# Optimization experiments

Measured on AMD Instinct MI355X. Metric: run time of the kernel, lower is better.

The kernel has to match this reference:

```python
import jax, jax.numpy as jnp
import numpy as np

ALPHA = 0.2          # LeakyReLU negative slope
NEG_FILL = -9e15     # mask value used by the original module


def setup_inputs() -> dict:
    key = jax.random.key(0)
    k1, k2, k3, k4 = jax.random.split(key, 4)
    N, D, H, F = 4096, 512, 8, 64  # nhid*nheads == embedding_dim
    h = jax.random.normal(k1, (N, D), dtype=jnp.float32)
    adj = jax.random.randint(k2, (N, N), 0, 2, dtype=jnp.int32)
    # per-head linear projection weights (no bias) and attention vectors
    W = jax.random.normal(k3, (H, D, F), dtype=jnp.float32) * (1.0 / np.sqrt(D))
    a = jax.random.normal(k4, (H, 2 * F), dtype=jnp.float32) * 0.1
    return {"h": h, "adj": adj, "W": W, "a": a}


def reference(h, adj, W, a):
    H, D, F = W.shape
    N = h.shape[0]
    # per-head projection: [H, N, F]
    hp = jnp.einsum('nd,hdf->hnf', h, W)
    # score(i,j) = leakyrelu(a[:F].h_i + a[F:].h_j)  (decomposed broadcast-add,
    # same math as the original N*N concat construction)
    a_src, a_dst = a[:, :F], a[:, F:]
    f_src = jnp.einsum('hnf,hf->hn', hp, a_src)  # [H, N]
    f_dst = jnp.einsum('hnf,hf->hn', hp, a_dst)  # [H, N]
    e = jax.nn.leaky_relu(f_src[:, :, None] + f_dst[:, None, :], ALPHA)  # [H,N,N]
    e = jnp.where(adj[None] > 0, e, NEG_FILL)
    att = jax.nn.softmax(e, axis=-1)  # softmax over neighbors j (dim=1 in torch)
    out = jnp.einsum('hij,hjf->hif', att, hp)  # [H, N, F]
    # concat heads -> [N, H*F], then ELU
    out = jnp.transpose(out, (1, 0, 2)).reshape(N, H * F)
    return jax.nn.elu(out)
```

## Files before the change

### kernel.cpp

```cpp
#include <hip/hip_runtime.h>

#define NN 4096
#define DD 512
#define HH 8
#define FF 64
#define LRELU_ALPHA 0.2f
#define SP 72
#define JSPLIT 2
#define JCHUNK (NN / JSPLIT)

typedef __attribute__((ext_vector_type(8))) short bf16x8;
typedef __attribute__((ext_vector_type(4))) float f32x4;

__device__ __forceinline__ float f4c(const float4& v, int k) {
    return k == 0 ? v.x : (k == 1 ? v.y : (k == 2 ? v.z : v.w));
}
__device__ __forceinline__ void f4s(float4& v, int k, float x) {
    if (k == 0) v.x = x; else if (k == 1) v.y = x; else if (k == 2) v.z = x; else v.w = x;
}
__device__ __forceinline__ unsigned short f2bf(float x) {
    unsigned u = __float_as_uint(x);
    return (unsigned short)((u + 0x7fffu + ((u >> 16) & 1u)) >> 16);
}
__device__ __forceinline__ float bf2f(unsigned short h) {
    return __uint_as_float(((unsigned)h) << 16);
}
__device__ __forceinline__ unsigned fkey(float x) {
    unsigned u = __float_as_uint(x);
    return (u & 0x80000000u) ? ~u : (u | 0x80000000u);
}
__device__ __forceinline__ float funkey(unsigned k) {
    unsigned u = (k & 0x80000000u) ? (k ^ 0x80000000u) : ~k;
    return __uint_as_float(u);
}

__global__ __launch_bounds__(256) void k_prep(const int* __restrict__ adj,
                                              const float* __restrict__ W,
                                              const float* __restrict__ hmat,
                                              unsigned long long* __restrict__ adjm,
                                              unsigned short* __restrict__ wt_hi,
                                              unsigned short* __restrict__ wt_lo,
                                              unsigned short* __restrict__ h_hi,
                                              unsigned short* __restrict__ h_lo,
                                              unsigned* __restrict__ mxkey,
                                              float* __restrict__ hpsum) {
    __shared__ unsigned long long shbuf[2080];
    int b = blockIdx.x, t = threadIdx.x;
    if (b < 2048) {
        int g = b >> 3, cs = b & 7;
        int r0 = g * 16;
        int lane = t & 63, wv = t >> 6;
        unsigned long long (*w64)[9] = (unsigned long long(*)[9])shbuf;
        for (int r = 0; r < 16; r++) {
            #pragma unroll
            for (int q = 0; q < 2; q++) {
                int col = cs * 512 + q * 256 + t;
                unsigned long long m = __ballot(adj[(size_t)(r0 + r) * NN + col] > 0);
                if (lane == 0) w64[r][q * 4 + wv] = m;
            }
        }
        __syncthreads();
        for (int tl = wv; tl < 8; tl += 4) {
            unsigned long long wbits = w64[lane & 15][tl];
            unsigned long long my = 0;
            #pragma unroll
            for (int k = 0; k < 16; k++) {
                int shv = 32 * (k >> 3) + 8 * (lane >> 4) + (k & 7);
                unsigned long long bal = __ballot((unsigned)((wbits >> shv) & 1ULL));
                if (lane == k) my = bal;
            }
            if (lane < 16)
                adjm[((size_t)g * 64 + cs * 8 + tl) * 16 + lane] = my;
        }
    } else if (b < 2112) {
        float (*tile)[65] = (float(*)[65])shbuf;
        int idx = b - 2048;
        int h = idx >> 3;
        int d0 = (idx & 7) * 64;
        #pragma unroll
        for (int kidx = 0; kidx < 4; kidx++) {
            int id = t + 256 * kidx;
            int dd = id >> 4, f4i = (id & 15) * 4;
            float4 v = *(const float4*)(W + ((size_t)(h * DD + d0 + dd)) * FF + f4i);
            tile[dd][f4i] = v.x; tile[dd][f4i + 1] = v.y;
            tile[dd][f4i + 2] = v.z; tile[dd][f4i + 3] = v.w;
        }
        __syncthreads();
        int f = t >> 2, c = (t & 3) * 16;
        union { unsigned short s[16]; uint4 v[2]; } hb, lb;
        #pragma unroll
        for (int q = 0; q < 16; q++) {
            float v = tile[c + q][f];
            unsigned short hi = f2bf(v);
            hb.s[q] = hi;
            lb.s[q] = f2bf(v - bf2f(hi));
        }
        uint4* dh = (uint4*)(wt_hi + ((size_t)h * FF + f) * DD + d0 + c);
        uint4* dl = (uint4*)(wt_lo + ((size_t)h * FF + f) * DD + d0 + c);
        dh[0] = hb.v[0]; dh[1] = hb.v[1];
        dl[0] = lb.v[0]; dl[1] = lb.v[1];
    } else if (b < 2368) {
        int idx = b - 2112;
        int row = idx * 16 + (t >> 4);
        int c0 = (t & 15) * 32;
        const float* src = hmat + (size_t)row * DD + c0;
        #pragma unroll
        for (int half = 0; half < 2; half++) {
            float4 p0 = *(const float4*)(src + half * 16);
            float4 p1 = *(const float4*)(src + half * 16 + 4);
            float4 p2 = *(const float4*)(src + half * 16 + 8);
            float4 p3 = *(const float4*)(src + half * 16 + 12);
            union { unsigned short s[16]; uint4 v[2]; } hb, lb;
            #pragma unroll
            for (int q = 0; q < 16; q++) {
                float v = q < 4 ? f4c(p0, q) : q < 8 ? f4c(p1, q - 4)
                          : q < 12 ? f4c(p2, q - 8) : f4c(p3, q - 12);
                unsigned short hi = f2bf(v);
                hb.s[q] = hi;
                lb.s[q] = f2bf(v - bf2f(hi));
            }
            uint4* dh = (uint4*)(h_hi + (size_t)row * DD + c0 + half * 16);
            uint4* dl = (uint4*)(h_lo + (size_t)row * DD + c0 + half * 16);
            dh[0] = hb.v[0]; dh[1] = hb.v[1];
            dl[0] = lb.v[0]; dl[1] = lb.v[1];
        }
    } else {
        if (t < 16) mxkey[t] = 0u;
        hpsum[t] = 0.f;
        hpsum[t + 256] = 0.f;
    }
}

__global__ __launch_bounds__(256) void k_hp_mfma(const unsigned short* __restrict__ hhi,
                                                 const unsigned short* __restrict__ hlo,
                                                 const unsigned short* __restrict__ whi,
                                                 const unsigned short* __restrict__ wlo,
                                                 const float* __restrict__ a,
                                                 unsigned short* __restrict__ hpT_hi,
                                                 float* __restrict__ fs,
                                                 float* __restrict__ fd,
                                                 float* __restrict__ hpsum,
                                                 unsigned* __restrict__ mxkey) {
    __shared__ char smem[4 * 64 * SP * 2];
    unsigned short* ah = (unsigned short*)smem;
    unsigned short* al = ah + 64 * SP;
    unsigned short* bh = al + 64 * SP;
    unsigned short* bl = bh + 64 * SP;

    int t = threadIdx.x;
    int h = blockIdx.y;
    int n0 = blockIdx.x * 64;
    int lane = t & 63;
    int w = t >> 6;
    int R0 = (w >> 1) * 32, F0 = (w & 1) * 32;
    int am = lane & 15, aq = lane >> 4;
    int sr = t >> 2, sc = (t & 3) * 16;

    const unsigned short* ghh = hhi + (size_t)(n0 + sr) * DD;
    const unsigned short* ghl = hlo + (size_t)(n0 + sr) * DD;
    const unsigned short* gbh = whi + ((size_t)h * FF + sr) * DD;
    const unsigned short* gbl = wlo + ((size_t)h * FF + sr) * DD;

    f32x4 acc[2][2] = {};
    for (int kk = 0; kk < DD; kk += 64) {
        {
            const uint4* s0 = (const uint4*)(ghh + kk + sc);
            const uint4* s1 = (const uint4*)(ghl + kk + sc);
            uint4 h0 = s0[0], h1 = s0[1], l0 = s1[0], l1 = s1[1];
            *(uint4*)(ah + sr * SP + sc) = h0; *(uint4*)(ah + sr * SP + sc + 8) = h1;
            *(uint4*)(al + sr * SP + sc) = l0; *(uint4*)(al + sr * SP + sc + 8) = l1;
        }
        {
            const uint4* s2 = (const uint4*)(gbh + kk + sc);
            const uint4* s3 = (const uint4*)(gbl + kk + sc);
            uint4 w0 = s2[0], w1 = s2[1], x0 = s3[0], x1 = s3[1];
            *(uint4*)(bh + sr * SP + sc) = w0; *(uint4*)(bh + sr * SP + sc + 8) = w1;
            *(uint4*)(bl + sr * SP + sc) = x0; *(uint4*)(bl + sr * SP + sc + 8) = x1;
        }
        __syncthreads();
        #pragma unroll
        for (int k2 = 0; k2 < 2; k2++) {
            int ko = k2 * 32 + aq * 8;
            bf16x8 a0h = *(const bf16x8*)(ah + (R0 + am) * SP + ko);
            bf16x8 a1h = *(const bf16x8*)(ah + (R0 + 16 + am) * SP + ko);
            bf16x8 a0l = *(const bf16x8*)(al + (R0 + am) * SP + ko);
            bf16x8 a1l = *(const bf16x8*)(al + (R0 + 16 + am) * SP + ko);
            bf16x8 b0h = *(const bf16x8*)(bh + (F0 + am) * SP + ko);
            bf16x8 b1h = *(const bf16x8*)(bh + (F0 + 16 + am) * SP + ko);
            bf16x8 b0l = *(const bf16x8*)(bl + (F0 + am) * SP + ko);
            bf16x8 b1l = *(const bf16x8*)(bl + (F0 + 16 + am) * SP + ko);
            acc[0][0] = __builtin_amdgcn_mfma_f32_16x16x32_bf16(a0h, b0h, acc[0][0], 0, 0, 0);
            acc[0][1] = __builtin_amdgcn_mfma_f32_16x16x32_bf16(a0h, b1h, acc[0][1], 0, 0, 0);
            acc[1][0] = __builtin_amdgcn_mfma_f32_16x16x32_bf16(a1h, b0h, acc[1][0], 0, 0, 0);
            acc[1][1] = __builtin_amdgcn_mfma_f32_16x16x32_bf16(a1h, b1h, acc[1][1], 0, 0, 0);
            acc[0][0] = __builtin_amdgcn_mfma_f32_16x16x32_bf16(a0h, b0l, acc[0][0], 0, 0, 0);
            acc[0][1] = __builtin_amdgcn_mfma_f32_16x16x32_bf16(a0h, b1l, acc[0][1], 0, 0, 0);
            acc[1][0] = __builtin_amdgcn_mfma_f32_16x16x32_bf16(a1h, b0l, acc[1][0], 0, 0, 0);
            acc[1][1] = __builtin_amdgcn_mfma_f32_16x16x32_bf16(a1h, b1l, acc[1][1], 0, 0, 0);
            acc[0][0] = __builtin_amdgcn_mfma_f32_16x16x32_bf16(a0l, b0h, acc[0][0], 0, 0, 0);
            acc[0][1] = __builtin_amdgcn_mfma_f32_16x16x32_bf16(a0l, b1h, acc[0][1], 0, 0, 0);
            acc[1][0] = __builtin_amdgcn_mfma_f32_16x16x32_bf16(a1l, b0h, acc[1][0], 0, 0, 0);
            acc[1][1] = __builtin_amdgcn_mfma_f32_16x16x32_bf16(a1l, b1h, acc[1][1], 0, 0, 0);
        }
        __syncthreads();
    }

    unsigned* tt = (unsigned*)smem;
    float* rs = (float*)(smem + 17408);
    float* rd = rs + 256;
    float* ash = rd + 256;
    if (t < 128) ash[t] = a[h * 2 * FF + t];
    int col = lane & 15, rbase = (lane >> 4) * 4;
    #pragma unroll
    for (int m16 = 0; m16 < 2; m16++) {
        #pragma unroll
        for (int n16 = 0; n16 < 2; n16++) {
            #pragma unroll
            for (int r = 0; r < 4; r++) {
                int nl = R0 + m16 * 16 + rbase + r;
                int f = F0 + n16 * 16 + col;
                float v = acc[m16][n16][r];
                unsigned short hi = f2bf(v);
                unsigned short lo = f2bf(v - bf2f(hi));
                tt[f * 68 + nl] = (unsigned)hi | ((unsigned)lo << 16);
            }
        }
    }
    __syncthreads();
    {
        int f = t >> 2, c = (t & 3) * 16;
        union { unsigned short s[16]; uint4 v[2]; } hb;
        float csum = 0.f;
        #pragma unroll
        for (int q = 0; q < 16; q++) {
            unsigned u = tt[f * 68 + c + q];
            hb.s[q] = (unsigned short)(u & 0xffffu);
            csum += bf2f((unsigned short)(u & 0xffffu)) + bf2f((unsigned short)(u >> 16));
        }
        uint4* dh = (uint4*)(hpT_hi + ((size_t)h * FF + f) * NN + n0 + c);
        dh[0] = hb.v[0]; dh[1] = hb.v[1];
        csum += __shfl_xor(csum, 1);
        csum += __shfl_xor(csum, 2);
        if ((t & 3) == 0) unsafeAtomicAdd(hpsum + h * FF + f, csum);
    }
    {
        int n = t & 63, g = t >> 6;
        float fsp = 0.f, fdp = 0.f;
        #pragma unroll
        for (int q = 0; q < 16; q++) {
            int f = g * 16 + q;
            unsigned u = tt[f * 68 + n];
            float v = bf2f((unsigned short)(u & 0xffffu)) + bf2f((unsigned short)(u >> 16));
            fsp += v * ash[f];
            fdp += v * ash[64 + f];
        }
        rs[g * 64 + n] = fsp;
        rd[g * 64 + n] = fdp;
    }
    __syncthreads();
    if (t < 64) {
        const float LOG2E = 1.44269504f;
        float fdv = (rd[t] + rd[64 + t] + rd[128 + t] + rd[192 + t]) * LOG2E;
        fs[(size_t)h * NN + n0 + t] = (rs[t] + rs[64 + t] + rs[128 + t] + rs[192 + t]) * LOG2E;
        fd[(size_t)h * NN + n0 + t] = fdv;
        unsigned key = fkey(fdv);
        #pragma unroll
        for (int off = 32; off; off >>= 1) key = max(key, (unsigned)__shfl_xor((int)key, off));
        if (t == 0) atomicMax(mxkey + h, key);
    }
}

__global__ __launch_bounds__(512) void k_attn(const float* __restrict__ fs,
                                              const float* __restrict__ fd,
                                              const unsigned* __restrict__ mxkey,
                                              const unsigned long long* __restrict__ adjm,
                                              const unsigned short* __restrict__ hpT_hi,
                                              const float* __restrict__ hpsum,
                                              float* __restrict__ outp) {
    __shared__ unsigned short hbh[2][2][64 * SP];

    int t = threadIdx.x;
    int h = blockIdx.y;
    int i0 = blockIdx.x * 64;
    int lane = t & 63;
    int w = t >> 6;
    int h2 = w >> 2;
    int rg = w & 3;
    int am = lane & 15, aq = lane >> 4;
    int th = t >> 8;
    int ts = t & 255;
    int sr = ts >> 2, sc = (ts & 3) * 16;

    float mfdL = funkey(mxkey[h]);
    float fsv = fs[(size_t)h * NN + i0 + rg * 16 + am];
    float sL = fsv + mfdL;
    float mrL = fmaxf(sL, LRELU_ALPHA * sL);
    float Ai = fsv - mrL;
    float Ci = -0.8f * mrL;

    int rgu = __builtin_amdgcn_readfirstlane(rg);
    int h2u = __builtin_amdgcn_readfirstlane(h2);
    const unsigned long long* mbase = adjm + ((size_t)(blockIdx.x * 4 + rgu) * 64) * 16;
    const unsigned short* gH = hpT_hi + (size_t)h * FF * NN;
    const float* fdh = fd + (size_t)h * NN + (size_t)h2u * JCHUNK;

    f32x4 acc[4] = {};
    f32x4 accl = {};
    bf16x8 ones;
    #pragma unroll
    for (int i = 0; i < 8; i++) ones[i] = (short)0x3f80;

    auto stage_load = [&](int j0, uint4& v0, uint4& v1) {
        const uint4* s = (const uint4*)(gH + (size_t)sr * NN + th * JCHUNK + j0 + sc);
        v0 = s[0]; v1 = s[1];
    };
    auto stage_write = [&](int buf, uint4 v0, uint4 v1) {
        *(uint4*)(&hbh[buf][th][sr * SP + sc]) = v0;
        *(uint4*)(&hbh[buf][th][sr * SP + sc + 8]) = v1;
    };
    auto fd_load = [&](int j0, float4* p) {
        p[0] = *(const float4*)(fdh + j0 + aq * 8);
        p[1] = *(const float4*)(fdh + j0 + aq * 8 + 4);
        p[2] = *(const float4*)(fdh + j0 + 32 + aq * 8);
        p[3] = *(const float4*)(fdh + j0 + 32 + aq * 8 + 4);
    };
    auto mkfrag = [&](float4 p0, float4 p1, const unsigned long long* mk, int off) -> bf16x8 {
        unsigned eu[8];
        #pragma unroll
        for (int q = 0; q < 2; q++) {
            float4 pv = q ? p1 : p0;
            #pragma unroll
            for (int bq = 0; bq < 4; bq++) {
                float tv = Ai + f4c(pv, bq);
                float uv = __builtin_fmaf(LRELU_ALPHA, tv, Ci);
                float ev = __builtin_amdgcn_exp2f(fmaxf(tv, uv));
                unsigned r;
                asm("v_cndmask_b32 %0, 0, %1, %2"
                    : "=v"(r) : "v"(ev), "s"(mk[off + q * 4 + bq]));
                eu[q * 4 + bq] = r;
            }
        }
        union { unsigned u[4]; bf16x8 v; } pk;
        pk.u[0] = __builtin_amdgcn_perm(eu[1], eu[0], 0x07060302);
        pk.u[1] = __builtin_amdgcn_perm(eu[3], eu[2], 0x07060302);
        pk.u[2] = __builtin_amdgcn_perm(eu[5], eu[4], 0x07060302);
        pk.u[3] = __builtin_amdgcn_perm(eu[7], eu[6], 0x07060302);
        return pk.v;
    };

    bf16x8 Pc0, Pc1;
    {
        uint4 v0, v1; float4 pf[4];
        stage_load(0, v0, v1);
        fd_load(0, pf);
        unsigned long long mk[16];
        #pragma unroll
        for (int k = 0; k < 16; k++) mk[k] = mbase[(size_t)(h2u * 32) * 16 + k];
        Pc0 = mkfrag(pf[0], pf[1], mk, 0);
        Pc1 = mkfrag(pf[2], pf[3], mk, 8);
        stage_write(0, v0, v1);
        __syncthreads();
    }

    for (int j0 = 0; j0 < JCHUNK; j0 += 64) {
        int cur = (j0 >> 6) & 1;
        int jn = (j0 + 64) & (JCHUNK - 1);
        uint4 v0, v1; float4 pf[4];
        stage_load(jn, v0, v1);
        fd_load(jn, pf);
        unsigned long long mk[16];
        #pragma unroll
        for (int k = 0; k < 16; k++) mk[k] = mbase[(size_t)(h2u * 32 + (jn >> 6)) * 16 + k];

        #pragma unroll
        for (int k2 = 0; k2 < 2; k2++) {
            int ko = k2 * 32 + aq * 8;
            bf16x8 x0 = *(const bf16x8*)(&hbh[cur][h2][(am)      * SP + ko]);
            bf16x8 x1 = *(const bf16x8*)(&hbh[cur][h2][(am + 16) * SP + ko]);
            bf16x8 x2 = *(const bf16x8*)(&hbh[cur][h2][(am + 32) * SP + ko]);
            bf16x8 x3 = *(const bf16x8*)(&hbh[cur][h2][(am + 48) * SP + ko]);
            bf16x8 P = k2 ? Pc1 : Pc0;
            acc[0] = __builtin_amdgcn_mfma_f32_16x16x32_bf16(x0, P, acc[0], 0, 0, 0);
            acc[1] = __builtin_amdgcn_mfma_f32_16x16x32_bf16(x1, P, acc[1], 0, 0, 0);
            acc[2] = __builtin_amdgcn_mfma_f32_16x16x32_bf16(x2, P, acc[2], 0, 0, 0);
            acc[3] = __builtin_amdgcn_mfma_f32_16x16x32_bf16(x3, P, acc[3], 0, 0, 0);
            accl   = __builtin_amdgcn_mfma_f32_16x16x32_bf16(ones, P, accl, 0, 0, 0);
        }

        stage_write(cur ^ 1, v0, v1);
        Pc0 = mkfrag(pf[0], pf[1], mk, 0);
        Pc1 = mkfrag(pf[2], pf[3], mk, 8);
        __syncthreads();
    }

    float* cb = (float*)hbh;
    if (h2 == 1) {
        #pragma unroll
        for (int mf = 0; mf < 4; mf++)
            *(f32x4*)&cb[((rg * 4 + mf) * 64 + lane) * 4] = acc[mf];
        cb[4096 + rg * 64 + lane] = accl[0];
    }
    __syncthreads();
    if (h2 == 0) {
        #pragma unroll
        for (int mf = 0; mf < 4; mf++) {
            f32x4 o = *(const f32x4*)&cb[((rg * 4 + mf) * 64 + lane) * 4];
            acc[mf] += o;
        }
        float li = accl[0] + cb[4096 + rg * 64 + lane];
        const float invN = 1.0f / NN;
        float rl = 1.f / li;
        int row = i0 + rg * 16 + am;
        float* orow = outp + (size_t)row * (HH * FF) + h * FF;
        #pragma unroll
        for (int mf = 0; mf < 4; mf++) {
            float4 ov;
            #pragma unroll
            for (int r = 0; r < 4; r++) {
                int f = mf * 16 + aq * 4 + r;
                float v;
                if (li > 0.f) v = acc[mf][r] * rl;
                else          v = hpsum[h * FF + f] * invN;
                v = v > 0.f ? v : __expf(v) - 1.f;
                f4s(ov, r, v);
            }
            *(float4*)(orow + mf * 16 + aq * 4) = ov;
        }
    }
}

extern "C" void kernel_launch(void* const* d_in, const int* in_sizes, int n_in,
                              void* d_out, int out_size, void* d_ws, size_t ws_size,
                              hipStream_t stream) {
    const float* hmat = (const float*)d_in[0];
    const int*   adj  = (const int*)d_in[1];
    const float* W    = (const float*)d_in[2];
    const float* a    = (const float*)d_in[3];
    float* out = (float*)d_out;

    char* ws = (char*)d_ws;
    unsigned short* hpT_hi = (unsigned short*)(ws);
    unsigned long long* adjm = (unsigned long long*)(ws + (4u << 20));
    unsigned short* wt_hi  = (unsigned short*)(ws + (6u << 20));
    unsigned short* wt_lo  = (unsigned short*)(ws + (6u << 20) + (512u << 10));
    float* fs    = (float*)(ws + (7u << 20));
    float* fd    = (float*)(ws + (7u << 20) + (128u << 10));
    unsigned* mxkey = (unsigned*)(ws + (7u << 20) + (256u << 10));
    float* hpsum = (float*)(mxkey + 16);
    unsigned short* h_hi = (unsigned short*)(ws + (8u << 20));
    unsigned short* h_lo = (unsigned short*)(ws + (12u << 20));

    k_prep   <<<dim3(2369),          256, 0, stream>>>(adj, W, hmat, adjm, wt_hi, wt_lo,
                                                       h_hi, h_lo, mxkey, hpsum);
    k_hp_mfma<<<dim3(64, 8),         256, 0, stream>>>(h_hi, h_lo, wt_hi, wt_lo, a,
                                                       hpT_hi, fs, fd, hpsum, mxkey);
    k_attn   <<<dim3(NN / 64, HH),   512, 0, stream>>>(fs, fd, mxkey, adjm,
                                                       hpT_hi, hpsum, out);
}
```

Measured before the change: 175.2 us.

## Split attention over j across two grid slices and combine partials in a new kernel

```diff
diff --git a/kernel.cpp b/kernel.cpp
--- a/kernel.cpp
+++ b/kernel.cpp
@@ -6,8 +6,7 @@
 #define FF 64
 #define LRELU_ALPHA 0.2f
 #define SP 72
-#define JSPLIT 2
-#define JCHUNK (NN / JSPLIT)
+#define JH 1024
 
 typedef __attribute__((ext_vector_type(8))) short bf16x8;
 typedef __attribute__((ext_vector_type(4))) float f32x4;
@@ -275,13 +274,15 @@
                                               const unsigned* __restrict__ mxkey,
                                               const unsigned long long* __restrict__ adjm,
                                               const unsigned short* __restrict__ hpT_hi,
-                                              const float* __restrict__ hpsum,
-                                              float* __restrict__ outp) {
+                                              float* __restrict__ outp,
+                                              float* __restrict__ poacc,
+                                              float* __restrict__ pli) {
     __shared__ unsigned short hbh[2][2][64 * SP];
 
     int t = threadIdx.x;
     int h = blockIdx.y;
     int i0 = blockIdx.x * 64;
+    int z = blockIdx.z;
     int lane = t & 63;
     int w = t >> 6;
     int h2 = w >> 2;
@@ -302,7 +303,7 @@
     int h2u = __builtin_amdgcn_readfirstlane(h2);
     const unsigned long long* mbase = adjm + ((size_t)(blockIdx.x * 4 + rgu) * 64) * 16;
     const unsigned short* gH = hpT_hi + (size_t)h * FF * NN;
-    const float* fdh = fd + (size_t)h * NN + (size_t)h2u * JCHUNK;
+    const float* fdh = fd + (size_t)h * NN + (size_t)z * 2048 + (size_t)h2u * JH;
 
     f32x4 acc[4] = {};
     f32x4 accl = {};
@@ -311,7 +312,7 @@
     for (int i = 0; i < 8; i++) ones[i] = (short)0x3f80;
 
     auto stage_load = [&](int j0, uint4& v0, uint4& v1) {
-        const uint4* s = (const uint4*)(gH + (size_t)sr * NN + th * JCHUNK + j0 + sc);
+        const uint4* s = (const uint4*)(gH + (size_t)sr * NN + z * 2048 + th * JH + j0 + sc);
         v0 = s[0]; v1 = s[1];
     };
     auto stage_write = [&](int buf, uint4 v0, uint4 v1) {
@@ -354,23 +355,25 @@
         stage_load(0, v0, v1);
         fd_load(0, pf);
         unsigned long long mk[16];
-        #pragma unroll
-        for (int k = 0; k < 16; k++) mk[k] = mbase[(size_t)(h2u * 32) * 16 + k];
+        size_t jt = (size_t)(z * 32 + h2u * 16) * 16;
+        #pragma unroll
+        for (int k = 0; k < 16; k++) mk[k] = mbase[jt + k];
         Pc0 = mkfrag(pf[0], pf[1], mk, 0);
         Pc1 = mkfrag(pf[2], pf[3], mk, 8);
         stage_write(0, v0, v1);
         __syncthreads();
     }
 
-    for (int j0 = 0; j0 < JCHUNK; j0 += 64) {
+    for (int j0 = 0; j0 < JH; j0 += 64) {
         int cur = (j0 >> 6) & 1;
-        int jn = (j0 + 64) & (JCHUNK - 1);
+        int jn = (j0 + 64) & (JH - 1);
         uint4 v0, v1; float4 pf[4];
         stage_load(jn, v0, v1);
         fd_load(jn, pf);
         unsigned long long mk[16];
-        #pragma unroll
-        for (int k = 0; k < 16; k++) mk[k] = mbase[(size_t)(h2u * 32 + (jn >> 6)) * 16 + k];
+        size_t jt = (size_t)(z * 32 + h2u * 16 + (jn >> 6)) * 16;
+        #pragma unroll
+        for (int k = 0; k < 16; k++) mk[k] = mbase[jt + k];
 
         #pragma unroll
         for (int k2 = 0; k2 < 2; k2++) {
@@ -408,25 +411,42 @@
             acc[mf] += o;
         }
         float li = accl[0] + cb[4096 + rg * 64 + lane];
-        const float invN = 1.0f / NN;
+        int row = i0 + rg * 16 + am;
+        float* dst = (z == 0) ? outp : poacc;
+        float* drow = dst + (size_t)row * (HH * FF) + h * FF;
+        #pragma unroll
+        for (int mf = 0; mf < 4; mf++)
+            *(f32x4*)(drow + mf * 16 + aq * 4) = acc[mf];
+        if (aq == 0) pli[(size_t)z * NN * HH + (size_t)row * HH + h] = li;
+    }
+}
+
+__global__ __launch_bounds__(256) void k_comb(float* __restrict__ outp,
+                                              const float* __restrict__ poacc,
+                                              const float* __restrict__ pli,
+                                              const float* __restrict__ hpsum) {
+    int gid = blockIdx.x * 256 + threadIdx.x;
+    const float invN = 1.0f / NN;
+    float4 v0 = ((const float4*)outp)[gid];
+    float4 v1 = ((const float4*)poacc)[gid];
+    int rh = gid >> 4;
+    int h = rh & (HH - 1);
+    int f0 = (gid & 15) * 4;
+    float li = pli[rh] + pli[NN * HH + rh];
+    float4 o;
+    if (li > 0.f) {
         float rl = 1.f / li;
-        int row = i0 + rg * 16 + am;
-        float* orow = outp + (size_t)row * (HH * FF) + h * FF;
-        #pragma unroll
-        for (int mf = 0; mf < 4; mf++) {
-            float4 ov;
-            #pragma unroll
-            for (int r = 0; r < 4; r++) {
-                int f = mf * 16 + aq * 4 + r;
-                float v;
-                if (li > 0.f) v = acc[mf][r] * rl;
-                else          v = hpsum[h * FF + f] * invN;
-                v = v > 0.f ? v : __expf(v) - 1.f;
-                f4s(ov, r, v);
-            }
-            *(float4*)(orow + mf * 16 + aq * 4) = ov;
-        }
-    }
+        o.x = (v0.x + v1.x) * rl; o.y = (v0.y + v1.y) * rl;
+        o.z = (v0.z + v1.z) * rl; o.w = (v0.w + v1.w) * rl;
+    } else {
+        o.x = hpsum[h * FF + f0]     * invN; o.y = hpsum[h * FF + f0 + 1] * invN;
+        o.z = hpsum[h * FF + f0 + 2] * invN; o.w = hpsum[h * FF + f0 + 3] * invN;
+    }
+    o.x = o.x > 0.f ? o.x : __expf(o.x) - 1.f;
+    o.y = o.y > 0.f ? o.y : __expf(o.y) - 1.f;
+    o.z = o.z > 0.f ? o.z : __expf(o.z) - 1.f;
+    o.w = o.w > 0.f ? o.w : __expf(o.w) - 1.f;
+    ((float4*)outp)[gid] = o;
 }
 
 extern "C" void kernel_launch(void* const* d_in, const int* in_sizes, int n_in,
@@ -447,13 +467,16 @@
     float* fd    = (float*)(ws + (7u << 20) + (128u << 10));
     unsigned* mxkey = (unsigned*)(ws + (7u << 20) + (256u << 10));
     float* hpsum = (float*)(mxkey + 16);
+    float* pli   = (float*)(ws + (7u << 20) + (384u << 10));
     unsigned short* h_hi = (unsigned short*)(ws + (8u << 20));
     unsigned short* h_lo = (unsigned short*)(ws + (12u << 20));
-
-    k_prep   <<<dim3(2369),          256, 0, stream>>>(adj, W, hmat, adjm, wt_hi, wt_lo,
-                                                       h_hi, h_lo, mxkey, hpsum);
-    k_hp_mfma<<<dim3(64, 8),         256, 0, stream>>>(h_hi, h_lo, wt_hi, wt_lo, a,
-                                                       hpT_hi, fs, fd, hpsum, mxkey);
-    k_attn   <<<dim3(NN / 64, HH),   512, 0, stream>>>(fs, fd, mxkey, adjm,
-                                                       hpT_hi, hpsum, out);
-}
+    float* poacc = (float*)(ws + (8u << 20));
+
+    k_prep   <<<dim3(2369),            256, 0, stream>>>(adj, W, hmat, adjm, wt_hi, wt_lo,
+                                                         h_hi, h_lo, mxkey, hpsum);
+    k_hp_mfma<<<dim3(64, 8),           256, 0, stream>>>(h_hi, h_lo, wt_hi, wt_lo, a,
+                                                         hpT_hi, fs, fd, hpsum, mxkey);
+    k_attn   <<<dim3(NN / 64, HH, 2),  512, 0, stream>>>(fs, fd, mxkey, adjm,
+                                                         hpT_hi, out, poacc, pli);
+    k_comb   <<<dim3(NN * HH * FF / 1024), 256, 0, stream>>>(out, poacc, pli, hpsum);
+}
```

Result: slower. 192.5 us (+9.9%).

## Factor softmax exponentials into per-node terms and deepen attention prefetch pipeline

Applied to the files above, without the earlier changes.

```diff
diff --git a/kernel.cpp b/kernel.cpp
--- a/kernel.cpp
+++ b/kernel.cpp
@@ -6,8 +6,7 @@
 #define FF 64
 #define LRELU_ALPHA 0.2f
 #define SP 72
-#define JSPLIT 2
-#define JCHUNK (NN / JSPLIT)
+#define JCHUNK 2048
 
 typedef __attribute__((ext_vector_type(8))) short bf16x8;
 typedef __attribute__((ext_vector_type(4))) float f32x4;
@@ -138,7 +137,8 @@
                                                  const float* __restrict__ a,
                                                  unsigned short* __restrict__ hpT_hi,
                                                  float* __restrict__ fs,
-                                                 float* __restrict__ fd,
+                                                 float* __restrict__ ejs,
+                                                 float* __restrict__ fjs,
                                                  float* __restrict__ hpsum,
                                                  unsigned* __restrict__ mxkey) {
     __shared__ char smem[4 * 64 * SP * 2];
@@ -262,7 +262,8 @@
         const float LOG2E = 1.44269504f;
         float fdv = (rd[t] + rd[64 + t] + rd[128 + t] + rd[192 + t]) * LOG2E;
         fs[(size_t)h * NN + n0 + t] = (rs[t] + rs[64 + t] + rs[128 + t] + rs[192 + t]) * LOG2E;
-        fd[(size_t)h * NN + n0 + t] = fdv;
+        ejs[(size_t)h * NN + n0 + t] = __builtin_amdgcn_exp2f(fdv);
+        fjs[(size_t)h * NN + n0 + t] = __builtin_amdgcn_exp2f(LRELU_ALPHA * fdv);
         unsigned key = fkey(fdv);
         #pragma unroll
         for (int off = 32; off; off >>= 1) key = max(key, (unsigned)__shfl_xor((int)key, off));
@@ -271,7 +272,8 @@
 }
 
 __global__ __launch_bounds__(512) void k_attn(const float* __restrict__ fs,
-                                              const float* __restrict__ fd,
+                                              const float* __restrict__ ejs,
+                                              const float* __restrict__ fjs,
                                               const unsigned* __restrict__ mxkey,
                                               const unsigned long long* __restrict__ adjm,
                                               const unsigned short* __restrict__ hpT_hi,
@@ -295,14 +297,15 @@
     float fsv = fs[(size_t)h * NN + i0 + rg * 16 + am];
     float sL = fsv + mfdL;
     float mrL = fmaxf(sL, LRELU_ALPHA * sL);
-    float Ai = fsv - mrL;
-    float Ci = -0.8f * mrL;
+    float EA = __builtin_amdgcn_exp2f(fsv - mrL);
+    float EC = __builtin_amdgcn_exp2f(LRELU_ALPHA * fsv - mrL);
 
     int rgu = __builtin_amdgcn_readfirstlane(rg);
     int h2u = __builtin_amdgcn_readfirstlane(h2);
     const unsigned long long* mbase = adjm + ((size_t)(blockIdx.x * 4 + rgu) * 64) * 16;
     const unsigned short* gH = hpT_hi + (size_t)h * FF * NN;
-    const float* fdh = fd + (size_t)h * NN + (size_t)h2u * JCHUNK;
+    const float* ejh = ejs + (size_t)h * NN + (size_t)h2u * JCHUNK;
+    const float* fjh = fjs + (size_t)h * NN + (size_t)h2u * JCHUNK;
 
     f32x4 acc[4] = {};
     f32x4 accl = {};
@@ -318,25 +321,28 @@
         *(uint4*)(&hbh[buf][th][sr * SP + sc]) = v0;
         *(uint4*)(&hbh[buf][th][sr * SP + sc + 8]) = v1;
     };
-    auto fd_load = [&](int j0, float4* p) {
-        p[0] = *(const float4*)(fdh + j0 + aq * 8);
-        p[1] = *(const float4*)(fdh + j0 + aq * 8 + 4);
-        p[2] = *(const float4*)(fdh + j0 + 32 + aq * 8);
-        p[3] = *(const float4*)(fdh + j0 + 32 + aq * 8 + 4);
+    auto ejf_load = [&](int j0, float4* pe, float4* pf) {
+        pe[0] = *(const float4*)(ejh + j0 + aq * 8);
+        pe[1] = *(const float4*)(ejh + j0 + aq * 8 + 4);
+        pe[2] = *(const float4*)(ejh + j0 + 32 + aq * 8);
+        pe[3] = *(const float4*)(ejh + j0 + 32 + aq * 8 + 4);
+        pf[0] = *(const float4*)(fjh + j0 + aq * 8);
+        pf[1] = *(const float4*)(fjh + j0 + aq * 8 + 4);
+        pf[2] = *(const float4*)(fjh + j0 + 32 + aq * 8);
+        pf[3] = *(const float4*)(fjh + j0 + 32 + aq * 8 + 4);
     };
-    auto mkfrag = [&](float4 p0, float4 p1, const unsigned long long* mk, int off) -> bf16x8 {
+    auto mkfrag = [&](const float4* pe, const float4* pf,
+                      const unsigned long long* mk, int off) -> bf16x8 {
         unsigned eu[8];
         #pragma unroll
         for (int q = 0; q < 2; q++) {
-            float4 pv = q ? p1 : p0;
+            float4 ev4 = pe[q], fv4 = pf[q];
             #pragma unroll
             for (int bq = 0; bq < 4; bq++) {
-                float tv = Ai + f4c(pv, bq);
-                float uv = __builtin_fmaf(LRELU_ALPHA, tv, Ci);
-                float ev = __builtin_amdgcn_exp2f(fmaxf(tv, uv));
+                float e = fmaxf(EA * f4c(ev4, bq), EC * f4c(fv4, bq));
                 unsigned r;
                 asm("v_cndmask_b32 %0, 0, %1, %2"
-                    : "=v"(r) : "v"(ev), "s"(mk[off + q * 4 + bq]));
+                    : "=v"(r) : "v"(e), "s"(mk[off + q * 4 + bq]));
                 eu[q * 4 + bq] = r;
             }
         }
@@ -347,31 +353,7 @@
         pk.u[3] = __builtin_amdgcn_perm(eu[7], eu[6], 0x07060302);
         return pk.v;
     };
-
-    bf16x8 Pc0, Pc1;
-    {
-        uint4 v0, v1; float4 pf[4];
-        stage_load(0, v0, v1);
-        fd_load(0, pf);
-        unsigned long long mk[16];
-        #pragma unroll
-        for (int k = 0; k < 16; k++) mk[k] = mbase[(size_t)(h2u * 32) * 16 + k];
-        Pc0 = mkfrag(pf[0], pf[1], mk, 0);
-        Pc1 = mkfrag(pf[2], pf[3], mk, 8);
-        stage_write(0, v0, v1);
-        __syncthreads();
-    }
-
-    for (int j0 = 0; j0 < JCHUNK; j0 += 64) {
-        int cur = (j0 >> 6) & 1;
-        int jn = (j0 + 64) & (JCHUNK - 1);
-        uint4 v0, v1; float4 pf[4];
-        stage_load(jn, v0, v1);
-        fd_load(jn, pf);
-        unsigned long long mk[16];
-        #pragma unroll
-        for (int k = 0; k < 16; k++) mk[k] = mbase[(size_t)(h2u * 32 + (jn >> 6)) * 16 + k];
-
+    auto consume = [&](int cur, bf16x8 P0, bf16x8 P1) {
         #pragma unroll
         for (int k2 = 0; k2 < 2; k2++) {
             int ko = k2 * 32 + aq * 8;
@@ -379,18 +361,64 @@
             bf16x8 x1 = *(const bf16x8*)(&hbh[cur][h2][(am + 16) * SP + ko]);
             bf16x8 x2 = *(const bf16x8*)(&hbh[cur][h2][(am + 32) * SP + ko]);
             bf16x8 x3 = *(const bf16x8*)(&hbh[cur][h2][(am + 48) * SP + ko]);
-            bf16x8 P = k2 ? Pc1 : Pc0;
+            bf16x8 P = k2 ? P1 : P0;
             acc[0] = __builtin_amdgcn_mfma_f32_16x16x32_bf16(x0, P, acc[0], 0, 0, 0);
             acc[1] = __builtin_amdgcn_mfma_f32_16x16x32_bf16(x1, P, acc[1], 0, 0, 0);
             acc[2] = __builtin_amdgcn_mfma_f32_16x16x32_bf16(x2, P, acc[2], 0, 0, 0);
             acc[3] = __builtin_amdgcn_mfma_f32_16x16x32_bf16(x3, P, acc[3], 0, 0, 0);
             accl   = __builtin_amdgcn_mfma_f32_16x16x32_bf16(ones, P, accl, 0, 0, 0);
         }
-
-        stage_write(cur ^ 1, v0, v1);
-        Pc0 = mkfrag(pf[0], pf[1], mk, 0);
-        Pc1 = mkfrag(pf[2], pf[3], mk, 8);
+    };
+
+    bf16x8 Pc0, Pc1;
+    uint4 svA0, svA1, svB0, svB1;
+    float4 peA[4], pfA[4], peB[4], pfB[4];
+    unsigned long long mkA[16], mkB[16];
+
+    {
+        uint4 v0, v1; float4 pe0[4], pf0[4];
+        unsigned long long mk0[16];
+        stage_load(0, v0, v1);
+        ejf_load(0, pe0, pf0);
+        #pragma unroll
+        for (int k = 0; k < 16; k++) mk0[k] = mbase[(size_t)(h2u * 32) * 16 + k];
+        Pc0 = mkfrag(pe0, pf0, mk0, 0);
+        Pc1 = mkfrag(pe0 + 2, pf0 + 2, mk0, 8);
+        stage_write(0, v0, v1);
+        stage_load(64, svA0, svA1);
+        ejf_load(64, peA, pfA);
+        #pragma unroll
+        for (int k = 0; k < 16; k++) mkA[k] = mbase[(size_t)(h2u * 32 + 1) * 16 + k];
         __syncthreads();
+    }
+
+    for (int j0 = 0; j0 < JCHUNK; j0 += 128) {
+        {
+            stage_write(1, svA0, svA1);
+            int j2 = (j0 + 128) & (JCHUNK - 1);
+            stage_load(j2, svB0, svB1);
+            ejf_load(j2, peB, pfB);
+            #pragma unroll
+            for (int k = 0; k < 16; k++)
+                mkB[k] = mbase[(size_t)(h2u * 32 + (j2 >> 6)) * 16 + k];
+            consume(0, Pc0, Pc1);
+            Pc0 = mkfrag(peA, pfA, mkA, 0);
+            Pc1 = mkfrag(peA + 2, pfA + 2, mkA, 8);
+            __syncthreads();
+        }
+        {
+            stage_write(0, svB0, svB1);
+            int j3 = (j0 + 192) & (JCHUNK - 1);
+            stage_load(j3, svA0, svA1);
+            ejf_load(j3, peA, pfA);
+            #pragma unroll
+            for (int k = 0; k < 16; k++)
+                mkA[k] = mbase[(size_t)(h2u * 32 + (j3 >> 6)) * 16 + k];
+            consume(1, Pc0, Pc1);
+            Pc0 = mkfrag(peB, pfB, mkB, 0);
+            Pc1 = mkfrag(peB + 2, pfB + 2, mkB, 8);
+            __syncthreads();
+        }
     }
 
     float* cb = (float*)hbh;
@@ -444,16 +472,17 @@
     unsigned short* wt_hi  = (unsigned short*)(ws + (6u << 20));
     unsigned short* wt_lo  = (unsigned short*)(ws + (6u << 20) + (512u << 10));
     float* fs    = (float*)(ws + (7u << 20));
-    float* fd    = (float*)(ws + (7u << 20) + (128u << 10));
+    float* ejs   = (float*)(ws + (7u << 20) + (128u << 10));
     unsigned* mxkey = (unsigned*)(ws + (7u << 20) + (256u << 10));
     float* hpsum = (float*)(mxkey + 16);
+    float* fjs   = (float*)(ws + (7u << 20) + (384u << 10));
     unsigned short* h_hi = (unsigned short*)(ws + (8u << 20));
     unsigned short* h_lo = (unsigned short*)(ws + (12u << 20));
 
     k_prep   <<<dim3(2369),          256, 0, stream>>>(adj, W, hmat, adjm, wt_hi, wt_lo,
                                                        h_hi, h_lo, mxkey, hpsum);
     k_hp_mfma<<<dim3(64, 8),         256, 0, stream>>>(h_hi, h_lo, wt_hi, wt_lo, a,
-                                                       hpT_hi, fs, fd, hpsum, mxkey);
-    k_attn   <<<dim3(NN / 64, HH),   512, 0, stream>>>(fs, fd, mxkey, adjm,
+                                                       hpT_hi, fs, ejs, fjs, hpsum, mxkey);
+    k_attn   <<<dim3(NN / 64, HH),   512, 0, stream>>>(fs, ejs, fjs, mxkey, adjm,
                                                        hpT_hi, hpsum, out);
 }
```

After: 191.7 us. +9.4%, slower.
